# Kernel tuning notes

Hardware: AMD Instinct MI355X
Metric: run time of the kernel (lower is better)

Reference implementation:

```python
import jax, jax.numpy as jnp
import numpy as np

N, E = 50000, 800000
F_IN, F_OUT, H, F_EDGE = 256, 32, 8, 5
LEAKY_SLOPE = 0.2


def setup_inputs() -> dict:
    key = jax.random.key(0)
    ks = jax.random.split(key, 6)
    x = jax.random.normal(ks[0], (N, F_IN), dtype=jnp.float32)
    edge_index = jax.random.randint(ks[1], (2, E), 0, N, dtype=jnp.int64)
    edge_attr = jax.random.normal(ks[2], (E, F_EDGE), dtype=jnp.float32)
    degree_src = jax.random.randint(ks[3], (E,), 0, 64, dtype=jnp.int64)
    # Xavier-uniform params
    lim_W = float(np.sqrt(6.0 / (F_IN + F_OUT)))
    W = jax.random.uniform(ks[4], (H, F_IN, F_OUT), minval=-lim_W, maxval=lim_W, dtype=jnp.float32)
    A = 2 * F_OUT + F_EDGE
    lim_a = float(np.sqrt(6.0 / (H + A)))
    a = jax.random.uniform(ks[5], (H, A), minval=-lim_a, maxval=lim_a, dtype=jnp.float32)
    lim_e = float(np.sqrt(1.0 / F_EDGE))
    W_edge_w = jax.random.uniform(jax.random.fold_in(key, 7), (F_EDGE, F_EDGE), minval=-lim_e, maxval=lim_e, dtype=jnp.float32)
    return {"x": x, "edge_index": edge_index, "edge_attr": edge_attr,
            "degree_src": degree_src, "W": W, "a": a, "W_edge_w": W_edge_w}


def reference(x, edge_index, edge_attr, degree_src, W, a, W_edge_w):
    n = x.shape[0]
    h, f_out = W.shape[0], W.shape[2]
    src, dst = edge_index[0], edge_index[1]
    # per-head projection: (N, H, F_out)
    Wh = jnp.einsum('nf,hfo->nho', x, W)
    # split attention vector instead of materializing the concat
    a_src, a_dst, a_e = a[:, :f_out], a[:, f_out:2 * f_out], a[:, 2 * f_out:]
    ef = edge_attr @ W_edge_w.T                      # (E, F_edge)
    e = (jnp.einsum('eho,ho->eh', Wh[src], a_src)
         + jnp.einsum('eho,ho->eh', Wh[dst], a_dst)
         + ef @ a_e.T)                                # (E, H)
    e = jax.nn.leaky_relu(e, LEAKY_SLOPE)
    scale = 1.0 / jnp.sqrt(jnp.clip(degree_src.astype(jnp.float32), 1.0, None))
    e = e * scale[:, None]
    # segment softmax over src; torch scatter_reduce amax include_self=True with zeros init -> max includes 0
    e_max = jnp.maximum(jax.ops.segment_max(e, src, num_segments=n), 0.0)
    e_exp = jnp.exp(e - e_max[src])
    e_sum = jax.ops.segment_sum(e_exp, src, num_segments=n)
    alpha = e_exp / (e_sum[src] + 1e-16)             # (E, H)
    msg = Wh[dst] * alpha[:, :, None]                # (E, H, F_out)
    out = jax.ops.segment_sum(msg, src, num_segments=n)
    out = jax.nn.elu(out.reshape(n, h * f_out))
    return out, alpha
```

## Files before the change

### kernel.cpp

```cpp
#include <hip/hip_runtime.h>
#include <hip/hip_bf16.h>
#include <math.h>

#define NN 50000
#define NE 800000
#define FIN 256
#define FOUT 32
#define NH 8
#define FE 5
#define AROW 69

typedef float f32x4 __attribute__((ext_vector_type(4)));
typedef short bf16x8 __attribute__((ext_vector_type(8)));

static __device__ __forceinline__ unsigned short f2bf(float f) {
    unsigned u = __float_as_uint(f);
    unsigned r = (u + 0x7FFFu + ((u >> 16) & 1u)) >> 16;
    return (unsigned short)r;
}
static __device__ __forceinline__ float bf2f(unsigned short b) {
    return __uint_as_float(((unsigned)b) << 16);
}

__global__ void k_cmat(const float* __restrict__ a, const float* __restrict__ Wew,
                       float* __restrict__ C) {
    int t = threadIdx.x;
    if (t < NH * FE) {
        int h = t / FE, k = t % FE;
        float s = 0.f;
        for (int j = 0; j < FE; ++j) s += a[h * AROW + 2 * FOUT + j] * Wew[j * FE + k];
        C[t] = s;
    }
}

__global__ __launch_bounds__(256) void k_prepB(const float* __restrict__ W,
                                               unsigned short* __restrict__ Bh,
                                               unsigned short* __restrict__ Bl) {
    int c = blockIdx.x;
    int k = threadIdx.x;
    int h = c >> 5, o = c & 31;
    float f = W[(size_t)h * (FIN * FOUT) + (size_t)k * FOUT + o];
    unsigned short hi = f2bf(f);
    unsigned short lo = f2bf(f - bf2f(hi));
    Bh[c * 256 + k] = hi;
    Bl[c * 256 + k] = lo;
}

__global__ __launch_bounds__(256) void k_gemm_mfma(const float* __restrict__ x,
                                                   const unsigned short* __restrict__ Bh,
                                                   const unsigned short* __restrict__ Bl,
                                                   const float* __restrict__ a,
                                                   unsigned short* __restrict__ Whb,
                                                   float* __restrict__ s1,
                                                   float* __restrict__ s2, int nrows) {
    __shared__ __align__(16) unsigned short Ah[64 * 56];
    int t = threadIdx.x;
    int w = t >> 6, l = t & 63;
    int r = l & 15, blk = l >> 4;
    int row0 = blockIdx.x * 64;
    int c0 = w * 64;

    f32x4 acc[4][4];
#pragma unroll
    for (int i = 0; i < 4; ++i)
#pragma unroll
        for (int j = 0; j < 4; ++j) acc[i][j] = (f32x4)(0.f);

    int srow = t >> 2, skq = (t & 3) * 8;
    const size_t xrow = (size_t)(row0 + srow) * FIN;

    for (int k0 = 0; k0 < FIN; k0 += 32) {
        {
            float v[8];
            if (row0 + srow < nrows) {
                f32x4 u0 = *(const f32x4*)&x[xrow + k0 + skq];
                f32x4 u1 = *(const f32x4*)&x[xrow + k0 + skq + 4];
                v[0] = u0.x; v[1] = u0.y; v[2] = u0.z; v[3] = u0.w;
                v[4] = u1.x; v[5] = u1.y; v[6] = u1.z; v[7] = u1.w;
            } else {
#pragma unroll
                for (int e = 0; e < 8; ++e) v[e] = 0.f;
            }
            bf16x8 hi;
#pragma unroll
            for (int e = 0; e < 8; ++e) hi[e] = (short)f2bf(v[e]);
            *(bf16x8*)&Ah[srow * 56 + skq] = hi;
        }
        __syncthreads();
        bf16x8 ah[4];
#pragma unroll
        for (int rt = 0; rt < 4; ++rt)
            ah[rt] = *(const bf16x8*)&Ah[(rt * 16 + r) * 56 + blk * 8];
#pragma unroll
        for (int ct = 0; ct < 4; ++ct) {
            int c = c0 + ct * 16 + r;
            bf16x8 bh = *(const bf16x8*)&Bh[c * 256 + k0 + blk * 8];
            bf16x8 bl = *(const bf16x8*)&Bl[c * 256 + k0 + blk * 8];
#pragma unroll
            for (int rt = 0; rt < 4; ++rt) {
                acc[rt][ct] = __builtin_amdgcn_mfma_f32_16x16x32_bf16(ah[rt], bh, acc[rt][ct], 0, 0, 0);
                acc[rt][ct] = __builtin_amdgcn_mfma_f32_16x16x32_bf16(ah[rt], bl, acc[rt][ct], 0, 0, 0);
            }
        }
        __syncthreads();
    }

#pragma unroll
    for (int rt = 0; rt < 4; ++rt) {
#pragma unroll
        for (int reg = 0; reg < 4; ++reg) {
            int row = row0 + rt * 16 + blk * 4 + reg;
            if (row < nrows) {
#pragma unroll
                for (int ct = 0; ct < 4; ++ct)
                    Whb[(size_t)row * 256 + c0 + ct * 16 + r] = f2bf(acc[rt][ct][reg]);
            }
        }
    }
    int h0 = 2 * w, h1 = 2 * w + 1;
    float as0 = a[h0 * AROW + r],       as0b = a[h0 * AROW + 16 + r];
    float ad0 = a[h0 * AROW + 32 + r],  ad0b = a[h0 * AROW + 48 + r];
    float as1 = a[h1 * AROW + r],       as1b = a[h1 * AROW + 16 + r];
    float ad1 = a[h1 * AROW + 32 + r],  ad1b = a[h1 * AROW + 48 + r];
#pragma unroll
    for (int rt = 0; rt < 4; ++rt) {
#pragma unroll
        for (int reg = 0; reg < 4; ++reg) {
            float p10 = acc[rt][0][reg] * as0 + acc[rt][1][reg] * as0b;
            float p20 = acc[rt][0][reg] * ad0 + acc[rt][1][reg] * ad0b;
            float p11 = acc[rt][2][reg] * as1 + acc[rt][3][reg] * as1b;
            float p21 = acc[rt][2][reg] * ad1 + acc[rt][3][reg] * ad1b;
#pragma unroll
            for (int d = 1; d < 16; d <<= 1) {
                p10 += __shfl_xor(p10, d);
                p20 += __shfl_xor(p20, d);
                p11 += __shfl_xor(p11, d);
                p21 += __shfl_xor(p21, d);
            }
            int row = row0 + rt * 16 + blk * 4 + reg;
            if (r == 0 && row < nrows) {
                s1[row * NH + h0] = p10;
                s2[row * NH + h0] = p20;
                s1[row * NH + h1] = p11;
                s2[row * NH + h1] = p21;
            }
        }
    }
}

__global__ __launch_bounds__(256) void k_count(const int* __restrict__ ei,
                                               int* __restrict__ counts) {
    int e = blockIdx.x * 256 + threadIdx.x;
    if (e < NE) atomicAdd(&counts[ei[e]], 1);
}

__global__ __launch_bounds__(256) void k_scanA(const int* __restrict__ counts,
                                               int* __restrict__ part,
                                               int* __restrict__ bsums, int n) {
    __shared__ int lds[256];
    int t = threadIdx.x;
    int base = blockIdx.x * 1024;
    int i0 = base + t * 4;
    int v0 = (i0 + 0 < n) ? counts[i0 + 0] : 0;
    int v1 = (i0 + 1 < n) ? counts[i0 + 1] : 0;
    int v2 = (i0 + 2 < n) ? counts[i0 + 2] : 0;
    int v3 = (i0 + 3 < n) ? counts[i0 + 3] : 0;
    int l0 = v0, l1 = l0 + v1, l2 = l1 + v2, l3 = l2 + v3;
    lds[t] = l3;
    __syncthreads();
    for (int off = 1; off < 256; off <<= 1) {
        int val = lds[t];
        if (t >= off) val += lds[t - off];
        __syncthreads();
        lds[t] = val;
        __syncthreads();
    }
    int excl = (t == 0) ? 0 : lds[t - 1];
    if (i0 + 0 < n) part[i0 + 0] = excl;
    if (i0 + 1 < n) part[i0 + 1] = excl + l0;
    if (i0 + 2 < n) part[i0 + 2] = excl + l1;
    if (i0 + 3 < n) part[i0 + 3] = excl + l2;
    if (t == 255) bsums[blockIdx.x] = lds[255];
}

__global__ void k_scanB(const int* __restrict__ bsums, int* __restrict__ boffs, int nb) {
    if (threadIdx.x == 0) {
        int run = 0;
        for (int b = 0; b < nb; ++b) { boffs[b] = run; run += bsums[b]; }
    }
}

__global__ __launch_bounds__(256) void k_scanC(int* __restrict__ row_ptr,
                                               const int* __restrict__ boffs, int n, int total) {
    int i = blockIdx.x * 256 + threadIdx.x;
    if (i < n) row_ptr[i] += boffs[i >> 10];
    else if (i == n) row_ptr[n] = total;
}

__global__ __launch_bounds__(256) void k_scatlog(const int* __restrict__ ei,
                                                 const float* __restrict__ eattr,
                                                 const int* __restrict__ degs,
                                                 const float* __restrict__ s1,
                                                 const float* __restrict__ s2,
                                                 const float* __restrict__ C,
                                                 const int* __restrict__ row_ptr,
                                                 int* __restrict__ fill,
                                                 float* __restrict__ e_perm,
                                                 int2* __restrict__ de_perm) {
    __shared__ float Cl[NH * FE];
    int t = threadIdx.x;
    if (t < NH * FE) Cl[t] = C[t];
    __syncthreads();
    int e = blockIdx.x * 256 + t;
    if (e >= NE) return;
    int src = ei[e], dst = ei[NE + e];
    int dg = degs[e];
    float scale = rsqrtf((float)(dg > 1 ? dg : 1));
    float ea0 = eattr[(size_t)e * FE + 0];
    float ea1 = eattr[(size_t)e * FE + 1];
    float ea2 = eattr[(size_t)e * FE + 2];
    float ea3 = eattr[(size_t)e * FE + 3];
    float ea4 = eattr[(size_t)e * FE + 4];
    float4 s1a = *(const float4*)&s1[src * NH];
    float4 s1b = *(const float4*)&s1[src * NH + 4];
    float4 s2a = *(const float4*)&s2[dst * NH];
    float4 s2b = *(const float4*)&s2[dst * NH + 4];
    float vs1[8] = {s1a.x, s1a.y, s1a.z, s1a.w, s1b.x, s1b.y, s1b.z, s1b.w};
    float vs2[8] = {s2a.x, s2a.y, s2a.z, s2a.w, s2b.x, s2b.y, s2b.z, s2b.w};
    float v[8];
#pragma unroll
    for (int h = 0; h < NH; ++h) {
        float q = vs1[h] + vs2[h] + ea0 * Cl[h * FE + 0] + ea1 * Cl[h * FE + 1] +
                  ea2 * Cl[h * FE + 2] + ea3 * Cl[h * FE + 3] + ea4 * Cl[h * FE + 4];
        q = q > 0.f ? q : 0.2f * q;
        v[h] = q * scale;
    }
    int p = row_ptr[src] + atomicAdd(&fill[src], 1);
    *(float4*)&e_perm[(size_t)p * 8]     = make_float4(v[0], v[1], v[2], v[3]);
    *(float4*)&e_perm[(size_t)p * 8 + 4] = make_float4(v[4], v[5], v[6], v[7]);
    de_perm[p] = make_int2(dst, e);
}

__global__ __launch_bounds__(256) void k_smmsg(const int* __restrict__ row_ptr,
                                               const float* __restrict__ e_perm,
                                               const int2* __restrict__ de_perm,
                                               const unsigned short* __restrict__ Whb,
                                               float* __restrict__ out_alpha,
                                               float* __restrict__ out) {
    __shared__ float al[4][256];
    __shared__ int dl[4][32];
    __shared__ int el[4][32];
    int t = threadIdx.x;
    int w = t >> 6, l = t & 63;
    int n = blockIdx.x * 4 + w;
    if (n >= NN) return;
    int start = row_ptr[n], deg = row_ptr[n + 1] - start;
    int j = l >> 3, h = l & 7;

    float vc[4];
#pragma unroll
    for (int q = 0; q < 4; ++q) {
        int b = j + 8 * q;
        vc[q] = (b < deg) ? e_perm[(size_t)(start + b) * 8 + h] : -1e30f;
    }
    float mx = 0.f;
#pragma unroll
    for (int q = 0; q < 4; ++q) mx = fmaxf(mx, vc[q]);
    for (int b = 32 + j; b < deg; b += 8)
        mx = fmaxf(mx, e_perm[(size_t)(start + b) * 8 + h]);
    mx = fmaxf(mx, __shfl_xor(mx, 8));
    mx = fmaxf(mx, __shfl_xor(mx, 16));
    mx = fmaxf(mx, __shfl_xor(mx, 32));
    float m = mx;
    float ex[4];
    float sm = 0.f;
#pragma unroll
    for (int q = 0; q < 4; ++q) { ex[q] = __expf(vc[q] - m); sm += ex[q]; }
    for (int b = 32 + j; b < deg; b += 8)
        sm += __expf(e_perm[(size_t)(start + b) * 8 + h] - m);
    sm += __shfl_xor(sm, 8);
    sm += __shfl_xor(sm, 16);
    sm += __shfl_xor(sm, 32);
    float inv = 1.f / (sm + 1e-16f);
    f32x4 acc = (f32x4)(0.f);
    int hh = l >> 3;
    for (int base = 0; base < deg; base += 32) {
        int cnt = deg - base;
        if (cnt > 32) cnt = 32;
        if (l < cnt) {
            int2 de = de_perm[start + base + l];
            dl[w][l] = de.x;
            el[w][l] = de.y;
        }
        asm volatile("s_waitcnt lgkmcnt(0)" ::: "memory");
#pragma unroll
        for (int q = 0; q < 4; ++q) {
            int b = base + j + 8 * q;
            if (b < deg) {
                float av = (base == 0 ? ex[q]
                                      : __expf(e_perm[(size_t)(start + b) * 8 + h] - m)) * inv;
                al[w][(j + 8 * q) * 8 + h] = av;
                out_alpha[(size_t)el[w][j + 8 * q] * 8 + h] = av;
            }
        }
        asm volatile("s_waitcnt lgkmcnt(0)" ::: "memory");
        for (int jj = 0; jj < cnt; ++jj) {
            int d = dl[w][jj];
            float av = al[w][jj * 8 + hh];
            ushort4 u = *(const ushort4*)&Whb[(size_t)d * 256 + l * 4];
            acc.x += av * bf2f(u.x);
            acc.y += av * bf2f(u.y);
            acc.z += av * bf2f(u.z);
            acc.w += av * bf2f(u.w);
        }
        asm volatile("s_waitcnt lgkmcnt(0)" ::: "memory");
    }
    f32x4 o;
    o.x = acc.x > 0.f ? acc.x : expm1f(acc.x);
    o.y = acc.y > 0.f ? acc.y : expm1f(acc.y);
    o.z = acc.z > 0.f ? acc.z : expm1f(acc.z);
    o.w = acc.w > 0.f ? acc.w : expm1f(acc.w);
    *(f32x4*)&out[(size_t)n * 256 + l * 4] = o;
}

extern "C" void kernel_launch(void* const* d_in, const int* in_sizes, int n_in,
                              void* d_out, int out_size, void* d_ws, size_t ws_size,
                              hipStream_t stream) {
    const float* x     = (const float*)d_in[0];
    const int*   ei    = (const int*)d_in[1];
    const float* eattr = (const float*)d_in[2];
    const int*   degs  = (const int*)d_in[3];
    const float* W     = (const float*)d_in[4];
    const float* a     = (const float*)d_in[5];
    const float* Wew   = (const float*)d_in[6];

    float* out       = (float*)d_out;
    float* out_alpha = out + (size_t)NN * 256;

    char* p = (char*)d_ws;
    auto alloc = [&](size_t bytes) -> char* {
        char* r = p;
        p += (bytes + 255) & ~(size_t)255;
        return r;
    };
    unsigned short* Whb     = (unsigned short*)alloc((size_t)NN * 256 * 2);
    float*          s1      = (float*)alloc((size_t)NN * NH * 4);
    float*          s2      = (float*)alloc((size_t)NN * NH * 4);
    float*          Cm      = (float*)alloc(NH * FE * 4);
    unsigned short* Bh      = (unsigned short*)alloc((size_t)256 * 256 * 2);
    unsigned short* Bl      = (unsigned short*)alloc((size_t)256 * 256 * 2);
    int*            counts  = (int*)alloc((size_t)NN * 4);
    int*            row_ptr = (int*)alloc((size_t)(NN + 1) * 4);
    int*            fill    = (int*)alloc((size_t)NN * 4);
    int*            bsums   = (int*)alloc(64 * 4);
    int*            boffs   = (int*)alloc(64 * 4);
    float*          e_perm  = (float*)alloc((size_t)NE * NH * 4);
    int2*           de_perm = (int2*)alloc((size_t)NE * 8);

    hipMemsetAsync(counts, 0, (size_t)NN * 4, stream);
    hipMemsetAsync(fill, 0, (size_t)NN * 4, stream);

    k_cmat<<<1, 64, 0, stream>>>(a, Wew, Cm);
    k_prepB<<<256, 256, 0, stream>>>(W, Bh, Bl);
    k_gemm_mfma<<<(NN + 63) / 64, 256, 0, stream>>>(x, Bh, Bl, a, Whb, s1, s2, NN);
    k_count<<<(NE + 255) / 256, 256, 0, stream>>>(ei, counts);
    k_scanA<<<(NN + 1023) / 1024, 256, 0, stream>>>(counts, row_ptr, bsums, NN);
    k_scanB<<<1, 64, 0, stream>>>(bsums, boffs, (NN + 1023) / 1024);
    k_scanC<<<(NN + 1 + 255) / 256, 256, 0, stream>>>(row_ptr, boffs, NN, NE);
    k_scatlog<<<(NE + 255) / 256, 256, 0, stream>>>(ei, eattr, degs, s1, s2, Cm,
                                                    row_ptr, fill, e_perm, de_perm);
    k_smmsg<<<(NN + 3) / 4, 256, 0, stream>>>(row_ptr, e_perm, de_perm, Whb,
                                              out_alpha, out);
}
```

Measured before the change: 235.4 us.

## Fuse prep kernels, fold attention vectors into GEMM, store edge logits as bf16

```diff
diff --git a/kernel.cpp b/kernel.cpp
--- a/kernel.cpp
+++ b/kernel.cpp
@@ -22,37 +22,59 @@
     return __uint_as_float(((unsigned)b) << 16);
 }
 
-__global__ void k_cmat(const float* __restrict__ a, const float* __restrict__ Wew,
-                       float* __restrict__ C) {
-    int t = threadIdx.x;
-    if (t < NH * FE) {
-        int h = t / FE, k = t % FE;
-        float s = 0.f;
-        for (int j = 0; j < FE; ++j) s += a[h * AROW + 2 * FOUT + j] * Wew[j * FE + k];
-        C[t] = s;
-    }
-}
-
-__global__ __launch_bounds__(256) void k_prepB(const float* __restrict__ W,
-                                               unsigned short* __restrict__ Bh,
-                                               unsigned short* __restrict__ Bl) {
-    int c = blockIdx.x;
-    int k = threadIdx.x;
-    int h = c >> 5, o = c & 31;
-    float f = W[(size_t)h * (FIN * FOUT) + (size_t)k * FOUT + o];
-    unsigned short hi = f2bf(f);
-    unsigned short lo = f2bf(f - bf2f(hi));
-    Bh[c * 256 + k] = hi;
-    Bl[c * 256 + k] = lo;
+__global__ __launch_bounds__(256) void k_prep(const float* __restrict__ W,
+                                              const float* __restrict__ a,
+                                              const float* __restrict__ Wew,
+                                              float* __restrict__ C,
+                                              unsigned short* __restrict__ Bh,
+                                              unsigned short* __restrict__ Bl,
+                                              unsigned short* __restrict__ Bsh,
+                                              unsigned short* __restrict__ Bsl) {
+    int t = threadIdx.x;
+    if (blockIdx.x == 0) {
+        if (t < NH * FE) {
+            int h = t / FE, k = t % FE;
+            float s = 0.f;
+            for (int j = 0; j < FE; ++j) s += a[h * AROW + 2 * FOUT + j] * Wew[j * FE + k];
+            C[t] = s;
+        }
+        int k = t;
+        for (int h = 0; h < NH; ++h) {
+            float s1v = 0.f, s2v = 0.f;
+            for (int o = 0; o < FOUT; ++o) {
+                float wv = W[(size_t)h * (FIN * FOUT) + (size_t)k * FOUT + o];
+                s1v += wv * a[h * AROW + o];
+                s2v += wv * a[h * AROW + FOUT + o];
+            }
+            unsigned short h1 = f2bf(s1v);
+            Bsh[h * 256 + k] = h1;
+            Bsl[h * 256 + k] = f2bf(s1v - bf2f(h1));
+            unsigned short h2 = f2bf(s2v);
+            Bsh[(8 + h) * 256 + k] = h2;
+            Bsl[(8 + h) * 256 + k] = f2bf(s2v - bf2f(h2));
+        }
+    } else {
+        int c = blockIdx.x - 1;
+        int k = t;
+        int h = c >> 5, o = c & 31;
+        float f = W[(size_t)h * (FIN * FOUT) + (size_t)k * FOUT + o];
+        unsigned short hi = f2bf(f);
+        unsigned short lo = f2bf(f - bf2f(hi));
+        Bh[c * 256 + k] = hi;
+        Bl[c * 256 + k] = lo;
+    }
 }
 
 __global__ __launch_bounds__(256) void k_gemm_mfma(const float* __restrict__ x,
                                                    const unsigned short* __restrict__ Bh,
                                                    const unsigned short* __restrict__ Bl,
-                                                   const float* __restrict__ a,
+                                                   const unsigned short* __restrict__ Bsh,
+                                                   const unsigned short* __restrict__ Bsl,
                                                    unsigned short* __restrict__ Whb,
                                                    float* __restrict__ s1,
-                                                   float* __restrict__ s2, int nrows) {
+                                                   float* __restrict__ s2,
+                                                   const int* __restrict__ ei,
+                                                   int* __restrict__ counts, int nrows) {
     __shared__ __align__(16) unsigned short Ah[64 * 56];
     int t = threadIdx.x;
     int w = t >> 6, l = t & 63;
@@ -61,6 +83,7 @@
     int c0 = w * 64;
 
     f32x4 acc[4][4];
+    f32x4 acc_s = (f32x4)(0.f);
 #pragma unroll
     for (int i = 0; i < 4; ++i)
 #pragma unroll
@@ -102,6 +125,12 @@
                 acc[rt][ct] = __builtin_amdgcn_mfma_f32_16x16x32_bf16(ah[rt], bl, acc[rt][ct], 0, 0, 0);
             }
         }
+        {
+            bf16x8 bsh = *(const bf16x8*)&Bsh[r * 256 + k0 + blk * 8];
+            bf16x8 bsl = *(const bf16x8*)&Bsl[r * 256 + k0 + blk * 8];
+            acc_s = __builtin_amdgcn_mfma_f32_16x16x32_bf16(ah[w], bsh, acc_s, 0, 0, 0);
+            acc_s = __builtin_amdgcn_mfma_f32_16x16x32_bf16(ah[w], bsl, acc_s, 0, 0, 0);
+        }
         __syncthreads();
     }
 
@@ -117,41 +146,25 @@
             }
         }
     }
-    int h0 = 2 * w, h1 = 2 * w + 1;
-    float as0 = a[h0 * AROW + r],       as0b = a[h0 * AROW + 16 + r];
-    float ad0 = a[h0 * AROW + 32 + r],  ad0b = a[h0 * AROW + 48 + r];
-    float as1 = a[h1 * AROW + r],       as1b = a[h1 * AROW + 16 + r];
-    float ad1 = a[h1 * AROW + 32 + r],  ad1b = a[h1 * AROW + 48 + r];
-#pragma unroll
-    for (int rt = 0; rt < 4; ++rt) {
-#pragma unroll
-        for (int reg = 0; reg < 4; ++reg) {
-            float p10 = acc[rt][0][reg] * as0 + acc[rt][1][reg] * as0b;
-            float p20 = acc[rt][0][reg] * ad0 + acc[rt][1][reg] * ad0b;
-            float p11 = acc[rt][2][reg] * as1 + acc[rt][3][reg] * as1b;
-            float p21 = acc[rt][2][reg] * ad1 + acc[rt][3][reg] * ad1b;
-#pragma unroll
-            for (int d = 1; d < 16; d <<= 1) {
-                p10 += __shfl_xor(p10, d);
-                p20 += __shfl_xor(p20, d);
-                p11 += __shfl_xor(p11, d);
-                p21 += __shfl_xor(p21, d);
-            }
-            int row = row0 + rt * 16 + blk * 4 + reg;
-            if (r == 0 && row < nrows) {
-                s1[row * NH + h0] = p10;
-                s2[row * NH + h0] = p20;
-                s1[row * NH + h1] = p11;
-                s2[row * NH + h1] = p21;
-            }
-        }
-    }
-}
-
-__global__ __launch_bounds__(256) void k_count(const int* __restrict__ ei,
-                                               int* __restrict__ counts) {
-    int e = blockIdx.x * 256 + threadIdx.x;
-    if (e < NE) atomicAdd(&counts[ei[e]], 1);
+#pragma unroll
+    for (int reg = 0; reg < 4; ++reg) {
+        int row = row0 + w * 16 + blk * 4 + reg;
+        if (row < nrows) {
+            if (r < 8) s1[row * NH + r] = acc_s[reg];
+            else       s2[row * NH + (r - 8)] = acc_s[reg];
+        }
+    }
+    int e0 = (blockIdx.x * 256 + t) * 4;
+    if (e0 + 3 < NE) {
+        int4 e4 = *(const int4*)&ei[e0];
+        atomicAdd(&counts[e4.x], 1);
+        atomicAdd(&counts[e4.y], 1);
+        atomicAdd(&counts[e4.z], 1);
+        atomicAdd(&counts[e4.w], 1);
+    } else {
+        for (int q = 0; q < 4; ++q)
+            if (e0 + q < NE) atomicAdd(&counts[ei[e0 + q]], 1);
+    }
 }
 
 __global__ __launch_bounds__(256) void k_scanA(const int* __restrict__ counts,
@@ -184,10 +197,19 @@
 }
 
 __global__ void k_scanB(const int* __restrict__ bsums, int* __restrict__ boffs, int nb) {
-    if (threadIdx.x == 0) {
-        int run = 0;
-        for (int b = 0; b < nb; ++b) { boffs[b] = run; run += bsums[b]; }
-    }
+    __shared__ int s[64];
+    int t = threadIdx.x;
+    int v = (t < nb) ? bsums[t] : 0;
+    s[t] = v;
+    __syncthreads();
+    for (int off = 1; off < 64; off <<= 1) {
+        int x = s[t];
+        if (t >= off) x += s[t - off];
+        __syncthreads();
+        s[t] = x;
+        __syncthreads();
+    }
+    if (t < nb) boffs[t] = s[t] - v;
 }
 
 __global__ __launch_bounds__(256) void k_scanC(int* __restrict__ row_ptr,
@@ -204,8 +226,8 @@
                                                  const float* __restrict__ s2,
                                                  const float* __restrict__ C,
                                                  const int* __restrict__ row_ptr,
-                                                 int* __restrict__ fill,
-                                                 float* __restrict__ e_perm,
+                                                 int* __restrict__ counts,
+                                                 unsigned short* __restrict__ e_perm,
                                                  int2* __restrict__ de_perm) {
     __shared__ float Cl[NH * FE];
     int t = threadIdx.x;
@@ -227,22 +249,22 @@
     float4 s2b = *(const float4*)&s2[dst * NH + 4];
     float vs1[8] = {s1a.x, s1a.y, s1a.z, s1a.w, s1b.x, s1b.y, s1b.z, s1b.w};
     float vs2[8] = {s2a.x, s2a.y, s2a.z, s2a.w, s2b.x, s2b.y, s2b.z, s2b.w};
-    float v[8];
+    bf16x8 v;
 #pragma unroll
     for (int h = 0; h < NH; ++h) {
         float q = vs1[h] + vs2[h] + ea0 * Cl[h * FE + 0] + ea1 * Cl[h * FE + 1] +
                   ea2 * Cl[h * FE + 2] + ea3 * Cl[h * FE + 3] + ea4 * Cl[h * FE + 4];
         q = q > 0.f ? q : 0.2f * q;
-        v[h] = q * scale;
-    }
-    int p = row_ptr[src] + atomicAdd(&fill[src], 1);
-    *(float4*)&e_perm[(size_t)p * 8]     = make_float4(v[0], v[1], v[2], v[3]);
-    *(float4*)&e_perm[(size_t)p * 8 + 4] = make_float4(v[4], v[5], v[6], v[7]);
+        v[h] = (short)f2bf(q * scale);
+    }
+    int old = atomicSub(&counts[src], 1);
+    int p = row_ptr[src] + old - 1;
+    *(bf16x8*)&e_perm[(size_t)p * 8] = v;
     de_perm[p] = make_int2(dst, e);
 }
 
 __global__ __launch_bounds__(256) void k_smmsg(const int* __restrict__ row_ptr,
-                                               const float* __restrict__ e_perm,
+                                               const unsigned short* __restrict__ e_perm,
                                                const int2* __restrict__ de_perm,
                                                const unsigned short* __restrict__ Whb,
                                                float* __restrict__ out_alpha,
@@ -261,13 +283,13 @@
 #pragma unroll
     for (int q = 0; q < 4; ++q) {
         int b = j + 8 * q;
-        vc[q] = (b < deg) ? e_perm[(size_t)(start + b) * 8 + h] : -1e30f;
+        vc[q] = (b < deg) ? bf2f(e_perm[(size_t)(start + b) * 8 + h]) : -1e30f;
     }
     float mx = 0.f;
 #pragma unroll
     for (int q = 0; q < 4; ++q) mx = fmaxf(mx, vc[q]);
     for (int b = 32 + j; b < deg; b += 8)
-        mx = fmaxf(mx, e_perm[(size_t)(start + b) * 8 + h]);
+        mx = fmaxf(mx, bf2f(e_perm[(size_t)(start + b) * 8 + h]));
     mx = fmaxf(mx, __shfl_xor(mx, 8));
     mx = fmaxf(mx, __shfl_xor(mx, 16));
     mx = fmaxf(mx, __shfl_xor(mx, 32));
@@ -277,7 +299,7 @@
 #pragma unroll
     for (int q = 0; q < 4; ++q) { ex[q] = __expf(vc[q] - m); sm += ex[q]; }
     for (int b = 32 + j; b < deg; b += 8)
-        sm += __expf(e_perm[(size_t)(start + b) * 8 + h] - m);
+        sm += __expf(bf2f(e_perm[(size_t)(start + b) * 8 + h]) - m);
     sm += __shfl_xor(sm, 8);
     sm += __shfl_xor(sm, 16);
     sm += __shfl_xor(sm, 32);
@@ -298,7 +320,7 @@
             int b = base + j + 8 * q;
             if (b < deg) {
                 float av = (base == 0 ? ex[q]
-                                      : __expf(e_perm[(size_t)(start + b) * 8 + h] - m)) * inv;
+                                      : __expf(bf2f(e_perm[(size_t)(start + b) * 8 + h]) - m)) * inv;
                 al[w][(j + 8 * q) * 8 + h] = av;
                 out_alpha[(size_t)el[w][j + 8 * q] * 8 + h] = av;
             }
@@ -349,26 +371,25 @@
     float*          Cm      = (float*)alloc(NH * FE * 4);
     unsigned short* Bh      = (unsigned short*)alloc((size_t)256 * 256 * 2);
     unsigned short* Bl      = (unsigned short*)alloc((size_t)256 * 256 * 2);
+    unsigned short* Bsh     = (unsigned short*)alloc((size_t)16 * 256 * 2);
+    unsigned short* Bsl     = (unsigned short*)alloc((size_t)16 * 256 * 2);
     int*            counts  = (int*)alloc((size_t)NN * 4);
     int*            row_ptr = (int*)alloc((size_t)(NN + 1) * 4);
-    int*            fill    = (int*)alloc((size_t)NN * 4);
     int*            bsums   = (int*)alloc(64 * 4);
     int*            boffs   = (int*)alloc(64 * 4);
-    float*          e_perm  = (float*)alloc((size_t)NE * NH * 4);
+    unsigned short* e_perm  = (unsigned short*)alloc((size_t)NE * NH * 2);
     int2*           de_perm = (int2*)alloc((size_t)NE * 8);
 
     hipMemsetAsync(counts, 0, (size_t)NN * 4, stream);
-    hipMemsetAsync(fill, 0, (size_t)NN * 4, stream);
-
-    k_cmat<<<1, 64, 0, stream>>>(a, Wew, Cm);
-    k_prepB<<<256, 256, 0, stream>>>(W, Bh, Bl);
-    k_gemm_mfma<<<(NN + 63) / 64, 256, 0, stream>>>(x, Bh, Bl, a, Whb, s1, s2, NN);
-    k_count<<<(NE + 255) / 256, 256, 0, stream>>>(ei, counts);
+
+    k_prep<<<257, 256, 0, stream>>>(W, a, Wew, Cm, Bh, Bl, Bsh, Bsl);
+    k_gemm_mfma<<<(NN + 63) / 64, 256, 0, stream>>>(x, Bh, Bl, Bsh, Bsl, Whb, s1, s2,
+                                                    ei, counts, NN);
     k_scanA<<<(NN + 1023) / 1024, 256, 0, stream>>>(counts, row_ptr, bsums, NN);
     k_scanB<<<1, 64, 0, stream>>>(bsums, boffs, (NN + 1023) / 1024);
     k_scanC<<<(NN + 1 + 255) / 256, 256, 0, stream>>>(row_ptr, boffs, NN, NE);
     k_scatlog<<<(NE + 255) / 256, 256, 0, stream>>>(ei, eattr, degs, s1, s2, Cm,
-                                                    row_ptr, fill, e_perm, de_perm);
+                                                    row_ptr, counts, e_perm, de_perm);
     k_smmsg<<<(NN + 3) / 4, 256, 0, stream>>>(row_ptr, e_perm, de_perm, Whb,
                                               out_alpha, out);
 }
```

New measurement: 246.5 us. 4.7% more time.
